# Kernel optimization log

Hardware: AMD Instinct MI355X
Metric: run time of the kernel (lower is better)

The kernel has to match this reference:

```python
import jax, jax.numpy as jnp
import numpy as np

N_NODES = 20000
N_EDGES = 640000
NUM_FEATURES = 128
HIDDEN = 256
NUM_CLASSES = 40
EPS = 0.0  # GINConv default eps, not trained


def gin_conv(x, edge_index, W, b):
    # sum-aggregate neighbor features: messages flow src -> dst
    src, dst = edge_index[0], edge_index[1]
    agg = jax.ops.segment_sum(x[src], dst, num_segments=N_NODES)  # [N, d]
    h = (1.0 + EPS) * x + agg
    return h @ W + b


def setup_inputs() -> dict:
    key = jax.random.key(0)
    ks = jax.random.split(key, 10)
    x = jax.random.normal(ks[0], (N_NODES, NUM_FEATURES), dtype=jnp.float32)
    edge_index = jax.random.randint(ks[1], (2, N_EDGES), 0, N_NODES, dtype=jnp.int64)

    def lin(k, fan_in, fan_out):
        kw, kb = jax.random.split(k)
        lim = 1.0 / np.sqrt(fan_in)
        W = jax.random.uniform(kw, (fan_in, fan_out), jnp.float32, -lim, lim)
        b = jax.random.uniform(kb, (fan_out,), jnp.float32, -lim, lim)
        return W, b

    W1, b1 = lin(ks[2], NUM_FEATURES, HIDDEN)
    W2, b2 = lin(ks[3], HIDDEN, HIDDEN)
    W3, b3 = lin(ks[4], HIDDEN, HIDDEN)
    W4, b4 = lin(ks[5], HIDDEN, NUM_CLASSES)
    return {"x": x, "edge_index": edge_index,
            "W1": W1, "b1": b1, "W2": W2, "b2": b2,
            "W3": W3, "b3": b3, "W4": W4, "b4": b4}


def reference(x, edge_index, W1, b1, W2, b2, W3, b3, W4, b4):
    h = jax.nn.relu(gin_conv(x, edge_index, W1, b1))
    h = jax.nn.relu(gin_conv(h, edge_index, W2, b2))
    h = jax.nn.relu(gin_conv(h, edge_index, W3, b3))
    return gin_conv(h, edge_index, W4, b4)
```

## Files before the change

kernel.cpp:

```cpp
#include <hip/hip_runtime.h>

typedef __attribute__((ext_vector_type(8))) short bf16x8;
typedef __attribute__((ext_vector_type(4))) float f32x4;
typedef __attribute__((ext_vector_type(2))) float f32x2;

#define CAP 128
#define EB 4096
#define NBJ 320
#define BSH 6

__device__ __forceinline__ ushort f2bf(float f) {
    union { float f; uint u; } c; c.f = f;
    uint u = c.u;
    u += 0x7fffu + ((u >> 16) & 1u);
    return (ushort)(u >> 16);
}
__device__ __forceinline__ f32x2 up2(uint u) {
    union { uint u; float f; } lo, hi;
    lo.u = u << 16; hi.u = u & 0xffff0000u;
    f32x2 r; r.x = lo.f; r.y = hi.f; return r;
}
__device__ __forceinline__ void acc4(f32x2* a, uint4 v) {
    a[0] += up2(v.x); a[1] += up2(v.y); a[2] += up2(v.z); a[3] += up2(v.w);
}

__global__ __launch_bounds__(256) void fill_cvtA(
        const int* __restrict__ src, const int* __restrict__ dst,
        uint* __restrict__ region, ushort* __restrict__ cntA, int E, int nAB,
        const float* __restrict__ x, ushort* __restrict__ xb, int n4,
        const float* __restrict__ W1, ushort* __restrict__ W1T,
        const float* __restrict__ W2, ushort* __restrict__ W2T,
        const float* __restrict__ W3, ushort* __restrict__ W3T,
        const float* __restrict__ W4, ushort* __restrict__ W4T) {
    if ((int)blockIdx.x < nAB) {
        __shared__ uint lcnt[NBJ];
        int tid = threadIdx.x;
        for (int i = tid; i < NBJ; i += 256) lcnt[i] = 0;
        __syncthreads();
        int b = blockIdx.x;
        int e0 = b * EB;
        int eend = e0 + EB < E ? e0 + EB : E;
        for (int e = e0 + tid; e < eend; e += 256) {
            uint d = (uint)dst[e];
            uint s = (uint)src[e];
            uint j = d >> BSH;
            uint pos = atomicAdd(&lcnt[j], 1u);
            region[(((uint)b * NBJ + j) << 6) + pos] = (d << 16) | s;
        }
        __syncthreads();
        for (int i = tid; i < NBJ; i += 256) cntA[(uint)b * NBJ + i] = (ushort)lcnt[i];
        return;
    }
    int idx = ((int)blockIdx.x - nAB) * 256 + threadIdx.x;
    if (idx < n4) {
        float4 v = *(const float4*)&x[(size_t)idx * 4];
        ushort4 o; o.x = f2bf(v.x); o.y = f2bf(v.y); o.z = f2bf(v.z); o.w = f2bf(v.w);
        *(ushort4*)&xb[(size_t)idx * 4] = o;
        return;
    }
    int i = idx - n4;
    if (i < 32768) {
        int n = i & 255, k = i >> 8;
        W1T[n * 128 + k] = f2bf(W1[k * 256 + n]);
    } else if (i < 32768 + 65536) {
        int j = i - 32768; int n = j & 255, k = j >> 8;
        W2T[n * 256 + k] = f2bf(W2[k * 256 + n]);
    } else if (i < 32768 + 131072) {
        int j = i - 98304; int n = j & 255, k = j >> 8;
        W3T[n * 256 + k] = f2bf(W3[k * 256 + n]);
    } else if (i < 32768 + 131072 + 32768) {
        int j = i - 163840; int n = j & 127, k = j >> 7;
        W4T[n * 256 + k] = f2bf(n < 40 ? W4[k * 40 + n] : 0.f);
    }
}

__global__ __launch_bounds__(256) void buildB(
        const uint* __restrict__ region, const ushort* __restrict__ cntA,
        int* __restrict__ cnt, ushort* __restrict__ pcsr, int N, int nAB) {
    __shared__ uint lcnt[64];
    __shared__ ushort ca[NBJ];
    int j = blockIdx.x;
    int tid = threadIdx.x;
    if (tid < 64) lcnt[tid] = 0;
    for (int b = tid; b < nAB; b += 256) ca[b] = cntA[(uint)b * NBJ + j];
    __syncthreads();
    int sub = tid >> 6;
    int i = tid & 63;
    int nbb = (nAB + 3) >> 2;
    for (int bb = 0; bb < nbb; ++bb) {
        int b = bb * 4 + sub;
        if (b < nAB && i < (int)ca[b]) {
            uint ev = region[(((uint)b * NBJ + j) << 6) + i];
            uint d = ev >> 16;
            uint pos = atomicAdd(&lcnt[d & 63], 1u);
            pcsr[((size_t)d << 7) + pos] = (ushort)(ev & 0xffffu);
        }
    }
    __syncthreads();
    int node = (j << BSH) + tid;
    if (tid < 64 && node < N) cnt[node] = (int)lcnt[tid];
}

template <int D>
__global__ __launch_bounds__(256) void gather_chunk(
        const ushort* __restrict__ xb, const int* __restrict__ cnt,
        const ushort* __restrict__ pcsr, ushort* __restrict__ h, int N) {
    constexpr int CF = D / 4;
    constexpr int LPN = CF / 8;
    constexpr int NPB = 256 / LPN;
    constexpr int RS = (D == 256) ? 9 : 8;
    int chunk = blockIdx.x & 3;
    int t = threadIdx.x;
    int node = (blockIdx.x >> 2) * NPB + (t / LPN);
    if (node >= N) return;
    int l = t & (LPN - 1);
    uint fo2 = (uint)chunk * (CF * 2) + (uint)l * 16;
    const char* xc = (const char*)xb;
    char* hc = (char*)h;
    int deg = cnt[node];
    const ushort* crow = pcsr + ((size_t)node << 7);
    uint selfoff = ((uint)node << RS) + fo2;

    f32x2 a[4], b[4] = {}, c[4] = {}, d[4] = {};
    {
        uint4 sv = *(const uint4*)(xc + selfoff);
        a[0] = up2(sv.x); a[1] = up2(sv.y); a[2] = up2(sv.z); a[3] = up2(sv.w);
    }
    int e = 0;
    for (; e + 8 <= deg; e += 8) {
        uint s0 = crow[e],     s1 = crow[e + 1], s2 = crow[e + 2], s3 = crow[e + 3];
        uint s4 = crow[e + 4], s5 = crow[e + 5], s6 = crow[e + 6], s7 = crow[e + 7];
        uint4 v0 = *(const uint4*)(xc + (s0 << RS) + fo2);
        uint4 v1 = *(const uint4*)(xc + (s1 << RS) + fo2);
        uint4 v2 = *(const uint4*)(xc + (s2 << RS) + fo2);
        uint4 v3 = *(const uint4*)(xc + (s3 << RS) + fo2);
        uint4 v4 = *(const uint4*)(xc + (s4 << RS) + fo2);
        uint4 v5 = *(const uint4*)(xc + (s5 << RS) + fo2);
        uint4 v6 = *(const uint4*)(xc + (s6 << RS) + fo2);
        uint4 v7 = *(const uint4*)(xc + (s7 << RS) + fo2);
        acc4(a, v0); acc4(b, v1); acc4(c, v2); acc4(d, v3);
        acc4(a, v4); acc4(b, v5); acc4(c, v6); acc4(d, v7);
    }
    for (; e + 4 <= deg; e += 4) {
        uint s0 = crow[e], s1 = crow[e + 1], s2 = crow[e + 2], s3 = crow[e + 3];
        uint4 v0 = *(const uint4*)(xc + (s0 << RS) + fo2);
        uint4 v1 = *(const uint4*)(xc + (s1 << RS) + fo2);
        uint4 v2 = *(const uint4*)(xc + (s2 << RS) + fo2);
        uint4 v3 = *(const uint4*)(xc + (s3 << RS) + fo2);
        acc4(a, v0); acc4(b, v1); acc4(c, v2); acc4(d, v3);
    }
    for (; e < deg; ++e) {
        uint s = crow[e];
        uint4 v = *(const uint4*)(xc + (s << RS) + fo2);
        acc4(a, v);
    }
    #pragma unroll
    for (int i = 0; i < 4; ++i) a[i] += (b[i] + c[i]) + d[i];
    uint4 o;
    o.x = (uint)f2bf(a[0].x) | ((uint)f2bf(a[0].y) << 16);
    o.y = (uint)f2bf(a[1].x) | ((uint)f2bf(a[1].y) << 16);
    o.z = (uint)f2bf(a[2].x) | ((uint)f2bf(a[2].y) << 16);
    o.w = (uint)f2bf(a[3].x) | ((uint)f2bf(a[3].y) << 16);
    *(uint4*)(hc + selfoff) = o;
}

__global__ __launch_bounds__(256) void gather_out_kernel(
        const ushort* __restrict__ y, const int* __restrict__ cnt,
        const ushort* __restrict__ pcsr, const float* __restrict__ b,
        float* __restrict__ out, int N) {
    int node = blockIdx.x * 32 + (threadIdx.x >> 3);
    if (node >= N) return;
    int l = threadIdx.x & 7;
    uint fo2 = (uint)l * 16;
    const char* yc = (const char*)y;
    int deg = cnt[node];
    const ushort* crow = pcsr + ((size_t)node << 7);

    f32x2 a[4], bb[4] = {}, cc[4] = {}, dd[4] = {};
    {
        uint4 sv = *(const uint4*)(yc + ((uint)node << 7) + fo2);
        a[0] = up2(sv.x); a[1] = up2(sv.y); a[2] = up2(sv.z); a[3] = up2(sv.w);
    }
    int e = 0;
    for (; e + 4 <= deg; e += 4) {
        uint s0 = crow[e], s1 = crow[e + 1], s2 = crow[e + 2], s3 = crow[e + 3];
        uint4 v0 = *(const uint4*)(yc + (s0 << 7) + fo2);
        uint4 v1 = *(const uint4*)(yc + (s1 << 7) + fo2);
        uint4 v2 = *(const uint4*)(yc + (s2 << 7) + fo2);
        uint4 v3 = *(const uint4*)(yc + (s3 << 7) + fo2);
        acc4(a, v0); acc4(bb, v1); acc4(cc, v2); acc4(dd, v3);
    }
    for (; e < deg; ++e) {
        uint s = crow[e];
        uint4 v = *(const uint4*)(yc + (s << 7) + fo2);
        acc4(a, v);
    }
    #pragma unroll
    for (int i = 0; i < 4; ++i) a[i] += (bb[i] + cc[i]) + dd[i];

    if (l < 5) {
        int f = l * 8;
        float4 o0 = make_float4(a[0].x + b[f + 0], a[0].y + b[f + 1],
                                a[1].x + b[f + 2], a[1].y + b[f + 3]);
        float4 o1 = make_float4(a[2].x + b[f + 4], a[2].y + b[f + 5],
                                a[3].x + b[f + 6], a[3].y + b[f + 7]);
        *(float4*)&out[(size_t)node * 40 + f] = o0;
        *(float4*)&out[(size_t)node * 40 + f + 4] = o1;
    }
}

#define GBM 64
#define GBN 128
#define GBK 64
#define LDT 72

template <bool OUTF32, bool RELU>
__global__ __launch_bounds__(256) void mfma_gemm(
        const ushort* __restrict__ A, const ushort* __restrict__ BT,
        const float* __restrict__ bias, void* __restrict__ Cout,
        int M, int Ncols, int K, int Cld) {
    __shared__ __align__(16) ushort As[GBM * LDT];
    __shared__ __align__(16) ushort Bs[GBN * LDT];
    int tid = threadIdx.x;
    int lane = tid & 63;
    int wave = tid >> 6;
    int row0 = blockIdx.x * GBM;
    int col0 = blockIdx.y * GBN;
    int wr = (wave >> 1) * 32;
    int wc = (wave & 1) * 64;
    int sr = tid >> 3;
    int sc = (tid & 7) * 8;
    int rr = lane & 15;
    int kq = (lane >> 4) * 8;
    f32x4 acc[2][4] = {};

    for (int k0 = 0; k0 < K; k0 += GBK) {
        int4 a0 = *(const int4*)&A[(size_t)(row0 + sr) * K + k0 + sc];
        int4 a1 = *(const int4*)&A[(size_t)(row0 + sr + 32) * K + k0 + sc];
        int4 b0 = *(const int4*)&BT[(size_t)(col0 + sr) * K + k0 + sc];
        int4 b1 = *(const int4*)&BT[(size_t)(col0 + sr + 32) * K + k0 + sc];
        int4 b2 = *(const int4*)&BT[(size_t)(col0 + sr + 64) * K + k0 + sc];
        int4 b3 = *(const int4*)&BT[(size_t)(col0 + sr + 96) * K + k0 + sc];
        __syncthreads();
        *(int4*)&As[sr * LDT + sc] = a0;
        *(int4*)&As[(sr + 32) * LDT + sc] = a1;
        *(int4*)&Bs[sr * LDT + sc] = b0;
        *(int4*)&Bs[(sr + 32) * LDT + sc] = b1;
        *(int4*)&Bs[(sr + 64) * LDT + sc] = b2;
        *(int4*)&Bs[(sr + 96) * LDT + sc] = b3;
        __syncthreads();
        #pragma unroll
        for (int kk = 0; kk < 2; ++kk) {
            int kof = kk * 32 + kq;
            bf16x8 af[2], bfr[4];
            #pragma unroll
            for (int i = 0; i < 2; ++i)
                af[i] = *(const bf16x8*)&As[(wr + i * 16 + rr) * LDT + kof];
            #pragma unroll
            for (int j = 0; j < 4; ++j)
                bfr[j] = *(const bf16x8*)&Bs[(wc + j * 16 + rr) * LDT + kof];
            #pragma unroll
            for (int i = 0; i < 2; ++i)
                #pragma unroll
                for (int j = 0; j < 4; ++j)
                    acc[i][j] = __builtin_amdgcn_mfma_f32_16x16x32_bf16(af[i], bfr[j], acc[i][j], 0, 0, 0);
        }
    }

    int rq = (lane >> 4) * 4;
    #pragma unroll
    for (int j = 0; j < 4; ++j) {
        int col = col0 + wc + j * 16 + rr;
        if (col >= Ncols) continue;
        float bv = bias ? bias[col] : 0.f;
        #pragma unroll
        for (int i = 0; i < 2; ++i) {
            #pragma unroll
            for (int r = 0; r < 4; ++r) {
                int row = row0 + wr + i * 16 + rq + r;
                if (row >= M) continue;
                float v = acc[i][j][r] + bv;
                if (RELU) v = fmaxf(v, 0.f);
                if (OUTF32) ((float*)Cout)[(size_t)row * Cld + col] = v;
                else        ((ushort*)Cout)[(size_t)row * Cld + col] = f2bf(v);
            }
        }
    }
}

static inline size_t al256(size_t x) { return (x + 255) & ~(size_t)255; }

extern "C" void kernel_launch(void* const* d_in, const int* in_sizes, int n_in,
                              void* d_out, int out_size, void* d_ws, size_t ws_size,
                              hipStream_t stream) {
    const float* x  = (const float*)d_in[0];
    const int*   ei = (const int*)d_in[1];
    const float* W1 = (const float*)d_in[2];
    const float* b1 = (const float*)d_in[3];
    const float* W2 = (const float*)d_in[4];
    const float* b2 = (const float*)d_in[5];
    const float* W3 = (const float*)d_in[6];
    const float* b3 = (const float*)d_in[7];
    const float* W4 = (const float*)d_in[8];
    const float* b4 = (const float*)d_in[9];
    float* out = (float*)d_out;

    int N = in_sizes[0] / 128;
    int E = in_sizes[1] / 2;
    const int* src = ei;
    const int* dst = ei + E;
    int Mpad = ((N + 127) / 128) * 128;
    int nAB = (E + EB - 1) / EB;
    int NB  = (N + 63) >> BSH;

    char* ws = (char*)d_ws;
    int* cnt       = (int*)ws;
    ushort* pcsr   = (ushort*)(cnt + N);
    ushort* cntA   = pcsr + (size_t)N * CAP;
    uint* region   = (uint*)(cntA + (size_t)nAB * NBJ);
    size_t off = al256((size_t)N * 4 + (size_t)N * CAP * 2 +
                       (size_t)nAB * NBJ * 2 + (size_t)nAB * NBJ * 64 * 4);
    ushort* xb   = (ushort*)(ws + off); off += al256((size_t)N * 128 * 2);
    ushort* bufH = (ushort*)(ws + off); off += al256((size_t)Mpad * 256 * 2);
    ushort* bufA = (ushort*)(ws + off); off += al256((size_t)Mpad * 256 * 2);
    ushort* bufB = (ushort*)(ws + off); off += al256((size_t)Mpad * 256 * 2);
    ushort* bufY = (ushort*)(ws + off); off += al256((size_t)Mpad * 64 * 2);
    ushort* W1T  = (ushort*)(ws + off); off += al256((size_t)256 * 128 * 2);
    ushort* W2T  = (ushort*)(ws + off); off += al256((size_t)256 * 256 * 2);
    ushort* W3T  = (ushort*)(ws + off); off += al256((size_t)256 * 256 * 2);
    ushort* W4T  = (ushort*)(ws + off); off += al256((size_t)128 * 256 * 2);

    int n4 = N * 128 / 4;
    int cvtBlocks = (n4 + 196608 + 255) / 256;
    fill_cvtA<<<nAB + cvtBlocks, 256, 0, stream>>>(src, dst, region, cntA, E, nAB, x, xb, n4,
                                                   W1, W1T, W2, W2T, W3, W3T, W4, W4T);
    buildB<<<NB, 256, 0, stream>>>(region, cntA, cnt, pcsr, N, nAB);

    int g1Blocks = ((N + 63) / 64) * 4;
    int g2Blocks = ((N + 31) / 32) * 4;
    dim3 gemmGrid(Mpad / GBM, 2);
    dim3 gemmGrid4(Mpad / GBM, 1);

    gather_chunk<128><<<g1Blocks, 256, 0, stream>>>(xb, cnt, pcsr, bufH, N);
    mfma_gemm<false, true><<<gemmGrid, 256, 0, stream>>>(bufH, W1T, b1, bufA, N, 256, 128, 256);
    gather_chunk<256><<<g2Blocks, 256, 0, stream>>>(bufA, cnt, pcsr, bufH, N);
    mfma_gemm<false, true><<<gemmGrid, 256, 0, stream>>>(bufH, W2T, b2, bufB, N, 256, 256, 256);
    gather_chunk<256><<<g2Blocks, 256, 0, stream>>>(bufB, cnt, pcsr, bufH, N);
    mfma_gemm<false, true><<<gemmGrid, 256, 0, stream>>>(bufH, W3T, b3, bufA, N, 256, 256, 256);
    mfma_gemm<false, false><<<gemmGrid4, 256, 0, stream>>>(bufA, W4T, nullptr, bufY, N, 64, 256, 64);
    gather_out_kernel<<<(N + 31) / 32, 256, 0, stream>>>(bufY, cnt, pcsr, b4, out, N);
}
```

Measured before the change: 156.0 us.

## Fuse layer-3 GEMM with W4 projection and widen edge/gather loads

Replaces the separate layer-3 GEMM and W4 projection with one kernel. Each block computes a 64x256 relu tile, keeps it in shared memory as bf16, and multiplies it by W4T directly. This removes the intermediate global write and reread of the 256-wide hidden activations and one launch, at the cost of more shared memory and registers per block. The edge bucketing loop now reads src/dst in int2 pairs, and the output gather is unrolled to 8 neighbors per iteration for more memory-level parallelism.

```diff
diff --git a/kernel.cpp b/kernel.cpp
--- a/kernel.cpp
+++ b/kernel.cpp
@@ -8,6 +8,11 @@
 #define EB 4096
 #define NBJ 320
 #define BSH 6
+#define GBM 64
+#define GBN 128
+#define GBK 64
+#define LDT 72
+#define LDT2 264
 
 __device__ __forceinline__ ushort f2bf(float f) {
     union { float f; uint u; } c; c.f = f;
@@ -40,12 +45,15 @@
         int b = blockIdx.x;
         int e0 = b * EB;
         int eend = e0 + EB < E ? e0 + EB : E;
-        for (int e = e0 + tid; e < eend; e += 256) {
-            uint d = (uint)dst[e];
-            uint s = (uint)src[e];
-            uint j = d >> BSH;
-            uint pos = atomicAdd(&lcnt[j], 1u);
-            region[(((uint)b * NBJ + j) << 6) + pos] = (d << 16) | s;
+        for (int e = e0 + tid * 2; e < eend; e += 512) {
+            int2 dd = *(const int2*)&dst[e];
+            int2 ss = *(const int2*)&src[e];
+            uint j0 = (uint)dd.x >> BSH;
+            uint p0 = atomicAdd(&lcnt[j0], 1u);
+            region[(((uint)b * NBJ + j0) << 6) + p0] = ((uint)dd.x << 16) | (uint)ss.x;
+            uint j1 = (uint)dd.y >> BSH;
+            uint p1 = atomicAdd(&lcnt[j1], 1u);
+            region[(((uint)b * NBJ + j1) << 6) + p1] = ((uint)dd.y << 16) | (uint)ss.y;
         }
         __syncthreads();
         for (int i = tid; i < NBJ; i += 256) cntA[(uint)b * NBJ + i] = (ushort)lcnt[i];
@@ -182,6 +190,20 @@
         a[0] = up2(sv.x); a[1] = up2(sv.y); a[2] = up2(sv.z); a[3] = up2(sv.w);
     }
     int e = 0;
+    for (; e + 8 <= deg; e += 8) {
+        uint s0 = crow[e],     s1 = crow[e + 1], s2 = crow[e + 2], s3 = crow[e + 3];
+        uint s4 = crow[e + 4], s5 = crow[e + 5], s6 = crow[e + 6], s7 = crow[e + 7];
+        uint4 v0 = *(const uint4*)(yc + (s0 << 7) + fo2);
+        uint4 v1 = *(const uint4*)(yc + (s1 << 7) + fo2);
+        uint4 v2 = *(const uint4*)(yc + (s2 << 7) + fo2);
+        uint4 v3 = *(const uint4*)(yc + (s3 << 7) + fo2);
+        uint4 v4 = *(const uint4*)(yc + (s4 << 7) + fo2);
+        uint4 v5 = *(const uint4*)(yc + (s5 << 7) + fo2);
+        uint4 v6 = *(const uint4*)(yc + (s6 << 7) + fo2);
+        uint4 v7 = *(const uint4*)(yc + (s7 << 7) + fo2);
+        acc4(a, v0); acc4(bb, v1); acc4(cc, v2); acc4(dd, v3);
+        acc4(a, v4); acc4(bb, v5); acc4(cc, v6); acc4(dd, v7);
+    }
     for (; e + 4 <= deg; e += 4) {
         uint s0 = crow[e], s1 = crow[e + 1], s2 = crow[e + 2], s3 = crow[e + 3];
         uint4 v0 = *(const uint4*)(yc + (s0 << 7) + fo2);
@@ -208,11 +230,6 @@
         *(float4*)&out[(size_t)node * 40 + f + 4] = o1;
     }
 }
-
-#define GBM 64
-#define GBN 128
-#define GBK 64
-#define LDT 72
 
 template <bool OUTF32, bool RELU>
 __global__ __launch_bounds__(256) void mfma_gemm(
@@ -288,6 +305,92 @@
     }
 }
 
+__global__ __launch_bounds__(256) void gemm3_fused(
+        const ushort* __restrict__ A, const ushort* __restrict__ BT,
+        const float* __restrict__ bias, const ushort* __restrict__ W4T,
+        ushort* __restrict__ Y) {
+    __shared__ __align__(16) ushort smem[(64 + 256) * LDT];
+    ushort* As = smem;
+    ushort* Bs = smem + 64 * LDT;
+    int tid = threadIdx.x;
+    int lane = tid & 63;
+    int wave = tid >> 6;
+    int row0 = blockIdx.x * 64;
+    int wc = wave * 64;
+    int sr = tid >> 3;
+    int sc = (tid & 7) * 8;
+    int rr = lane & 15;
+    int kq = (lane >> 4) * 8;
+    const int K = 256;
+    f32x4 acc[4][4] = {};
+
+    for (int k0 = 0; k0 < K; k0 += GBK) {
+        int4 a0 = *(const int4*)&A[(size_t)(row0 + sr) * K + k0 + sc];
+        int4 a1 = *(const int4*)&A[(size_t)(row0 + sr + 32) * K + k0 + sc];
+        int4 bb[8];
+        #pragma unroll
+        for (int q = 0; q < 8; ++q)
+            bb[q] = *(const int4*)&BT[(size_t)(sr + 32 * q) * K + k0 + sc];
+        __syncthreads();
+        *(int4*)&As[sr * LDT + sc] = a0;
+        *(int4*)&As[(sr + 32) * LDT + sc] = a1;
+        #pragma unroll
+        for (int q = 0; q < 8; ++q)
+            *(int4*)&Bs[(sr + 32 * q) * LDT + sc] = bb[q];
+        __syncthreads();
+        #pragma unroll
+        for (int kk = 0; kk < 2; ++kk) {
+            int kof = kk * 32 + kq;
+            bf16x8 af[4], bfr[4];
+            #pragma unroll
+            for (int i = 0; i < 4; ++i)
+                af[i] = *(const bf16x8*)&As[(i * 16 + rr) * LDT + kof];
+            #pragma unroll
+            for (int j = 0; j < 4; ++j)
+                bfr[j] = *(const bf16x8*)&Bs[(wc + j * 16 + rr) * LDT + kof];
+            #pragma unroll
+            for (int i = 0; i < 4; ++i)
+                #pragma unroll
+                for (int j = 0; j < 4; ++j)
+                    acc[i][j] = __builtin_amdgcn_mfma_f32_16x16x32_bf16(af[i], bfr[j], acc[i][j], 0, 0, 0);
+        }
+    }
+
+    __syncthreads();
+    ushort* Zs = smem;
+    int rq = (lane >> 4) * 4;
+    #pragma unroll
+    for (int j = 0; j < 4; ++j) {
+        int col = wc + j * 16 + rr;
+        float bv = bias[col];
+        #pragma unroll
+        for (int i = 0; i < 4; ++i)
+            #pragma unroll
+            for (int r = 0; r < 4; ++r)
+                Zs[(i * 16 + rq + r) * LDT2 + col] = f2bf(fmaxf(acc[i][j][r] + bv, 0.f));
+    }
+    __syncthreads();
+
+    f32x4 acc2[4] = {};
+    int n = wave * 16 + rr;
+    #pragma unroll
+    for (int ks = 0; ks < 8; ++ks) {
+        bf16x8 bf = *(const bf16x8*)&W4T[(size_t)n * 256 + ks * 32 + kq];
+        #pragma unroll
+        for (int i = 0; i < 4; ++i) {
+            bf16x8 af = *(const bf16x8*)&Zs[(i * 16 + rr) * LDT2 + ks * 32 + kq];
+            acc2[i] = __builtin_amdgcn_mfma_f32_16x16x32_bf16(af, bf, acc2[i], 0, 0, 0);
+        }
+    }
+    #pragma unroll
+    for (int i = 0; i < 4; ++i)
+        #pragma unroll
+        for (int r = 0; r < 4; ++r) {
+            int row = row0 + i * 16 + rq + r;
+            Y[((size_t)row << 6) + wave * 16 + rr] = f2bf(acc2[i][r]);
+        }
+}
+
 static inline size_t al256(size_t x) { return (x + 255) & ~(size_t)255; }
 
 extern "C" void kernel_launch(void* const* d_in, const int* in_sizes, int n_in,
@@ -339,14 +442,12 @@
     int g1Blocks = ((N + 63) / 64) * 4;
     int g2Blocks = ((N + 31) / 32) * 4;
     dim3 gemmGrid(Mpad / GBM, 2);
-    dim3 gemmGrid4(Mpad / GBM, 1);
 
     gather_chunk<128><<<g1Blocks, 256, 0, stream>>>(xb, cnt, pcsr, bufH, N);
     mfma_gemm<false, true><<<gemmGrid, 256, 0, stream>>>(bufH, W1T, b1, bufA, N, 256, 128, 256);
     gather_chunk<256><<<g2Blocks, 256, 0, stream>>>(bufA, cnt, pcsr, bufH, N);
     mfma_gemm<false, true><<<gemmGrid, 256, 0, stream>>>(bufH, W2T, b2, bufB, N, 256, 256, 256);
     gather_chunk<256><<<g2Blocks, 256, 0, stream>>>(bufB, cnt, pcsr, bufH, N);
-    mfma_gemm<false, true><<<gemmGrid, 256, 0, stream>>>(bufH, W3T, b3, bufA, N, 256, 256, 256);
-    mfma_gemm<false, false><<<gemmGrid4, 256, 0, stream>>>(bufA, W4T, nullptr, bufY, N, 64, 256, 64);
+    gemm3_fused<<<Mpad / 64, 256, 0, stream>>>(bufH, W3T, b3, W4T, bufY);
     gather_out_kernel<<<(N + 31) / 32, 256, 0, stream>>>(bufY, cnt, pcsr, b4, out, N);
 }
```

Measured after the change: 157.5 us. No clear change (+0.9%).
